# Optimization experiments

Hardware: AMD Instinct MI355X
Metric: run time of the kernel (lower is better)

Reference implementation:

```python
import jax, jax.numpy as jnp
import numpy as np

N = 100000   # nodes
E = 1600000  # edges
D = 128      # input feature dim
H1, H2 = 128, 128    # GCN hidden sizes
M1, M2 = 256, 128    # MLP hidden sizes
BN_EPS = 1e-5


def setup_inputs() -> dict:
    key = jax.random.key(0)
    ks = jax.random.split(key, 20)
    x = jax.random.normal(ks[0], (N, D), dtype=jnp.float32)
    edge_index = jax.random.randint(ks[1], (2, E), 0, N, dtype=jnp.int32)

    def lin(k, fi, fo):
        s = 1.0 / np.sqrt(fi)
        return jax.random.uniform(k, (fi, fo), jnp.float32, -s, s)

    inp = {"x": x, "edge_index": edge_index}
    inp["Wg1"] = lin(ks[2], D, H1);  inp["bg1"] = jnp.zeros((H1,), jnp.float32)
    inp["g1"]  = jnp.ones((H1,), jnp.float32); inp["be1"] = jnp.zeros((H1,), jnp.float32)
    inp["Wg2"] = lin(ks[3], H1, H2); inp["bg2"] = jnp.zeros((H2,), jnp.float32)
    inp["g2"]  = jnp.ones((H2,), jnp.float32); inp["be2"] = jnp.zeros((H2,), jnp.float32)
    inp["Wm1"] = lin(ks[4], H2, M1); inp["bm1"] = jnp.zeros((M1,), jnp.float32)
    inp["g3"]  = jnp.ones((M1,), jnp.float32); inp["be3"] = jnp.zeros((M1,), jnp.float32)
    inp["Wm2"] = lin(ks[5], M1, M2); inp["bm2"] = jnp.zeros((M2,), jnp.float32)
    inp["g4"]  = jnp.ones((M2,), jnp.float32); inp["be4"] = jnp.zeros((M2,), jnp.float32)
    inp["Wo"]  = lin(ks[6], M2, 1);  inp["bo"]  = jnp.zeros((1,), jnp.float32)
    return inp


def batch_norm(x, gamma, beta):
    # training-mode BatchNorm1d over the node/batch axis, biased variance
    mean = jnp.mean(x, axis=0)
    var = jnp.mean((x - mean) ** 2, axis=0)
    return (x - mean) * jax.lax.rsqrt(var + BN_EPS) * gamma + beta


def gcn_conv(x, src, dst, W, b):
    # PyG GCNConv: add self-loops, sym-normalize, aggregate (xW) over edges
    h = x @ W                                              # [N, F_out]
    deg = jnp.zeros((N,), x.dtype).at[dst].add(1.0) + 1.0  # in-degree + self-loop
    dinv = jax.lax.rsqrt(deg)
    coef = (dinv[src] * dinv[dst])[:, None]                # [E, 1]
    agg = jax.ops.segment_sum(h[src] * coef, dst, num_segments=N)
    agg = agg + h * (dinv * dinv)[:, None]                 # self-loop term
    return agg + b


def reference(x, edge_index, Wg1, bg1, g1, be1, Wg2, bg2, g2, be2,
              Wm1, bm1, g3, be3, Wm2, bm2, g4, be4, Wo, bo):
    src, dst = edge_index[0], edge_index[1]
    # GCN blocks: relu(dropout(bn(conv(x)))); dropout is identity in eval
    h = jax.nn.relu(batch_norm(gcn_conv(x, src, dst, Wg1, bg1), g1, be1))
    h = jax.nn.relu(batch_norm(gcn_conv(h, src, dst, Wg2, bg2), g2, be2))
    # MLP blocks
    h = jax.nn.relu(batch_norm(h @ Wm1 + bm1, g3, be3))
    h = jax.nn.relu(batch_norm(h @ Wm2 + bm2, g4, be4))
    return jax.nn.sigmoid(h @ Wo + bo)
```

## Files before the change

kernel.cpp:

```cpp
#include <hip/hip_runtime.h>
#include <hip/hip_bf16.h>
#include <math.h>


__global__ void degree_kernel(const int* __restrict__ dst, int* __restrict__ deg, int E) {
    int i = blockIdx.x * blockDim.x + threadIdx.x;
    if (i < E) atomicAdd(&deg[dst[i]], 1);
}

__global__ void dinv_kernel(const int* __restrict__ deg, float* __restrict__ dinv, int N) {
    int i = blockIdx.x * blockDim.x + threadIdx.x;
    if (i < N) dinv[i] = rsqrtf((float)(deg[i] + 1));
}

__global__ void blocksum_kernel(const int* __restrict__ deg, int* __restrict__ bsum, int N) {
    __shared__ int sh[256];
    int tid = threadIdx.x;
    int base = blockIdx.x * 1024 + tid * 4;
    int s = 0;
    #pragma unroll
    for (int j = 0; j < 4; ++j) { int idx = base + j; if (idx < N) s += deg[idx]; }
    sh[tid] = s; __syncthreads();
    for (int off = 128; off > 0; off >>= 1) {
        if (tid < off) sh[tid] += sh[tid + off];
        __syncthreads();
    }
    if (tid == 0) bsum[blockIdx.x] = sh[0];
}

__global__ void scan_bsum_kernel(int* bsum, int nb) {
    if (threadIdx.x == 0 && blockIdx.x == 0) {
        int run = 0;
        for (int i = 0; i < nb; ++i) { int v = bsum[i]; bsum[i] = run; run += v; }
    }
}

__global__ void scanwrite_kernel(const int* __restrict__ deg, const int* __restrict__ bsumex,
                                 int* __restrict__ row_ptr, int* __restrict__ cursor,
                                 int N, int Etot) {
    __shared__ int sh[256];
    int tid = threadIdx.x;
    int base = blockIdx.x * 1024 + tid * 4;
    int v[4]; int tsum = 0;
    #pragma unroll
    for (int j = 0; j < 4; ++j) { int idx = base + j; v[j] = (idx < N) ? deg[idx] : 0; tsum += v[j]; }
    sh[tid] = tsum; __syncthreads();
    for (int off = 1; off < 256; off <<= 1) {
        int x = (tid >= off) ? sh[tid - off] : 0;
        __syncthreads();
        sh[tid] += x;
        __syncthreads();
    }
    int run = sh[tid] - tsum + bsumex[blockIdx.x];
    #pragma unroll
    for (int j = 0; j < 4; ++j) {
        int idx = base + j;
        if (idx < N) { row_ptr[idx] = run; cursor[idx] = run; }
        run += v[j];
    }
    if (blockIdx.x == 0 && tid == 0) row_ptr[N] = Etot;
}

__global__ void scatter_kernel(const int* __restrict__ src, const int* __restrict__ dst,
                               int* __restrict__ cursor, int* __restrict__ edge_src, int E) {
    int i = blockIdx.x * blockDim.x + threadIdx.x;
    if (i < E) {
        int d = dst[i];
        int pos = atomicAdd(&cursor[d], 1);
        edge_src[pos] = src[i];
    }
}

template<bool ACT>
__global__ __launch_bounds__(256)
void gemm_kernel(const float* __restrict__ A, const float* __restrict__ W,
                 float* __restrict__ C, int nrows, int K, int FO,
                 const float* __restrict__ scale, const float* __restrict__ shift)
{
    __shared__ float As[32][132];
    __shared__ float Ws[32][132];
    const int tid = threadIdx.x;
    const int row0 = blockIdx.x * 128;
    const int c0 = blockIdx.y * 128;
    const int tx = tid & 15, ty = tid >> 4;
    float acc[8][8];
    #pragma unroll
    for (int i = 0; i < 8; ++i)
        #pragma unroll
        for (int j = 0; j < 8; ++j) acc[i][j] = 0.f;

    for (int k0 = 0; k0 < K; k0 += 32) {
        #pragma unroll
        for (int p = 0; p < 4; ++p) {
            int q = p * 256 + tid;
            int r = q >> 3;
            int kq = (q & 7) * 4;
            int gr = row0 + r;
            float4 v = make_float4(0.f, 0.f, 0.f, 0.f);
            if (gr < nrows) {
                v = *(const float4*)&A[(size_t)gr * K + k0 + kq];
                if (ACT) {
                    float4 sc = *(const float4*)&scale[k0 + kq];
                    float4 sf = *(const float4*)&shift[k0 + kq];
                    v.x = fmaxf(fmaf(v.x, sc.x, sf.x), 0.f);
                    v.y = fmaxf(fmaf(v.y, sc.y, sf.y), 0.f);
                    v.z = fmaxf(fmaf(v.z, sc.z, sf.z), 0.f);
                    v.w = fmaxf(fmaf(v.w, sc.w, sf.w), 0.f);
                }
            }
            As[kq + 0][r] = v.x; As[kq + 1][r] = v.y;
            As[kq + 2][r] = v.z; As[kq + 3][r] = v.w;
        }
        #pragma unroll
        for (int p = 0; p < 4; ++p) {
            int q = p * 256 + tid;
            int r = q >> 5;
            int cq = (q & 31) * 4;
            *(float4*)&Ws[r][cq] = *(const float4*)&W[(size_t)(k0 + r) * FO + c0 + cq];
        }
        __syncthreads();
        #pragma unroll
        for (int kk = 0; kk < 32; ++kk) {
            float4 a0 = *(const float4*)&As[kk][ty * 4];
            float4 a1 = *(const float4*)&As[kk][64 + ty * 4];
            float4 b0 = *(const float4*)&Ws[kk][tx * 4];
            float4 b1 = *(const float4*)&Ws[kk][64 + tx * 4];
            float a[8] = {a0.x, a0.y, a0.z, a0.w, a1.x, a1.y, a1.z, a1.w};
            float b[8] = {b0.x, b0.y, b0.z, b0.w, b1.x, b1.y, b1.z, b1.w};
            #pragma unroll
            for (int i = 0; i < 8; ++i)
                #pragma unroll
                for (int j = 0; j < 8; ++j)
                    acc[i][j] = fmaf(a[i], b[j], acc[i][j]);
        }
        __syncthreads();
    }
    #pragma unroll
    for (int i = 0; i < 8; ++i) {
        int r = (i < 4) ? (ty * 4 + i) : (64 + ty * 4 + i - 4);
        int gr = row0 + r;
        if (gr < nrows) {
            float4 o0 = make_float4(acc[i][0], acc[i][1], acc[i][2], acc[i][3]);
            float4 o1 = make_float4(acc[i][4], acc[i][5], acc[i][6], acc[i][7]);
            *(float4*)&C[(size_t)gr * FO + c0 + tx * 4] = o0;
            *(float4*)&C[(size_t)gr * FO + c0 + 64 + tx * 4] = o1;
        }
    }
}

__global__ void agg_kernel(const float* __restrict__ T, float* __restrict__ Aout,
                           const float* __restrict__ dinv,
                           const int* __restrict__ row_ptr, const int* __restrict__ edge_src,
                           int nrows)
{
    int gw = (blockIdx.x * blockDim.x + threadIdx.x) >> 6;
    int lane = threadIdx.x & 63;
    int nw = (gridDim.x * blockDim.x) >> 6;
    int c = lane * 2;
    for (int i = gw; i < nrows; i += nw) {
        float di = dinv[i];
        int e0 = row_ptr[i], e1 = row_ptr[i + 1];
        float ax = 0.f, ay = 0.f;
        for (int e = e0; e < e1; ++e) {
            int s = edge_src[e];
            float ws = dinv[s];
            float2 v = *(const float2*)&T[(size_t)s * 128 + c];
            ax = fmaf(ws, v.x, ax);
            ay = fmaf(ws, v.y, ay);
        }
        float2 self = *(const float2*)&T[(size_t)i * 128 + c];
        float2 o;
        o.x = fmaf(di, ax, di * di * self.x);
        o.y = fmaf(di, ay, di * di * self.y);
        *(float2*)&Aout[(size_t)i * 128 + c] = o;
    }
}

__global__ void colstats_kernel(const float* __restrict__ X, int nrows, int F, int rpb,
                                float* __restrict__ colsum, float* __restrict__ colsq)
{
    __shared__ float ss[256], sq[256];
    int tid = threadIdx.x;
    int c = tid & (F - 1);
    int roff = tid / F;
    int rstep = 256 / F;
    int r0 = blockIdx.x * rpb;
    int r1 = min(nrows, r0 + rpb);
    float s = 0.f, q = 0.f;
    for (int r = r0 + roff; r < r1; r += rstep) {
        float v = X[(size_t)r * F + c];
        s += v; q += v * v;
    }
    ss[tid] = s; sq[tid] = q;
    __syncthreads();
    if (tid < F) {
        float S = ss[tid], Q = sq[tid];
        for (int k = tid + F; k < 256; k += F) { S += ss[k]; Q += sq[k]; }
        atomicAdd(&colsum[tid], S);
        atomicAdd(&colsq[tid], Q);
    }
}

__global__ void bnparam_kernel(const float* __restrict__ colsum, const float* __restrict__ colsq,
                               const float* __restrict__ g, const float* __restrict__ be,
                               float* __restrict__ scale, float* __restrict__ shift,
                               int F, float invN)
{
    int c = blockIdx.x * blockDim.x + threadIdx.x;
    if (c < F) {
        float mean = colsum[c] * invN;
        float var = colsq[c] * invN - mean * mean;
        float rs = rsqrtf(var + 1e-5f);
        float sc = g[c] * rs;
        scale[c] = sc;
        shift[c] = be[c] - mean * sc;
    }
}

__global__ void final_kernel(const float* __restrict__ A, const float* __restrict__ Wo,
                             const float* __restrict__ bo,
                             const float* __restrict__ scale, const float* __restrict__ shift,
                             float* __restrict__ out, int nrows)
{
    int gw = (blockIdx.x * blockDim.x + threadIdx.x) >> 6;
    int lane = threadIdx.x & 63;
    int nw = (gridDim.x * blockDim.x) >> 6;
    int c = lane * 2;
    float2 w = *(const float2*)&Wo[c];
    float2 sc = *(const float2*)&scale[c];
    float2 sf = *(const float2*)&shift[c];
    float bias = bo[0];
    for (int i = gw; i < nrows; i += nw) {
        float2 v = *(const float2*)&A[(size_t)i * 128 + c];
        float x = fmaxf(fmaf(v.x, sc.x, sf.x), 0.f) * w.x
                + fmaxf(fmaf(v.y, sc.y, sf.y), 0.f) * w.y;
        #pragma unroll
        for (int off = 32; off > 0; off >>= 1) x += __shfl_down(x, off);
        if (lane == 0) out[i] = 1.f / (1.f + expf(-(x + bias)));
    }
}

extern "C" void kernel_launch(void* const* d_in, const int* in_sizes, int n_in,
                              void* d_out, int out_size, void* d_ws, size_t ws_size,
                              hipStream_t stream)
{
    const float* x   = (const float*)d_in[0];
    const int* ei    = (const int*)d_in[1];
    const float* Wg1 = (const float*)d_in[2];
    const float* g1  = (const float*)d_in[4];
    const float* be1 = (const float*)d_in[5];
    const float* Wg2 = (const float*)d_in[6];
    const float* g2  = (const float*)d_in[8];
    const float* be2 = (const float*)d_in[9];
    const float* Wm1 = (const float*)d_in[10];
    const float* g3  = (const float*)d_in[12];
    const float* be3 = (const float*)d_in[13];
    const float* Wm2 = (const float*)d_in[14];
    const float* g4  = (const float*)d_in[16];
    const float* be4 = (const float*)d_in[17];
    const float* Wo  = (const float*)d_in[18];
    const float* bo  = (const float*)d_in[19];

    const int N = in_sizes[0] / 128;
    const int E = in_sizes[1] / 2;
    const int* srcv = ei;
    const int* dstv = ei + E;

    char* p = (char*)d_ws;
    auto alloc = [&](size_t bytes) { void* r = (void*)p; p += (bytes + 255) & ~(size_t)255; return r; };
    float* T       = (float*)alloc((size_t)N * 256 * 4);
    float* Abuf    = (float*)alloc((size_t)N * 128 * 4);
    int*   deg     = (int*)alloc((size_t)N * 4);
    float* dinv    = (float*)alloc((size_t)N * 4);
    int*   row_ptr = (int*)alloc((size_t)(N + 1) * 4);
    int*   cursor  = (int*)alloc((size_t)N * 4);
    int*   edge_src= (int*)alloc((size_t)E * 4);
    int*   bsum    = (int*)alloc(4096);
    float* colsum  = (float*)alloc(512 * 4);
    float* colsq   = colsum + 256;
    float* scale   = (float*)alloc(256 * 4);
    float* shift   = (float*)alloc(256 * 4);

    const int rpb = (N + 255) / 256;
    const float invN = 1.f / (float)N;

    hipMemsetAsync(deg, 0, (size_t)N * 4, stream);
    degree_kernel<<<(E + 255) / 256, 256, 0, stream>>>(dstv, deg, E);
    dinv_kernel<<<(N + 255) / 256, 256, 0, stream>>>(deg, dinv, N);
    int nb = (N + 1023) / 1024;
    blocksum_kernel<<<nb, 256, 0, stream>>>(deg, bsum, N);
    scan_bsum_kernel<<<1, 64, 0, stream>>>(bsum, nb);
    scanwrite_kernel<<<nb, 256, 0, stream>>>(deg, bsum, row_ptr, cursor, N, E);
    scatter_kernel<<<(E + 255) / 256, 256, 0, stream>>>(srcv, dstv, cursor, edge_src, E);

    dim3 gemm_g((N + 127) / 128, 1);
    dim3 gemm_g2((N + 127) / 128, 2);

    gemm_kernel<false><<<gemm_g, 256, 0, stream>>>(x, Wg1, T, N, 128, 128, nullptr, nullptr);
    agg_kernel<<<2048, 256, 0, stream>>>(T, Abuf, dinv, row_ptr, edge_src, N);
    hipMemsetAsync(colsum, 0, 512 * 4, stream);
    colstats_kernel<<<256, 256, 0, stream>>>(Abuf, N, 128, rpb, colsum, colsq);
    bnparam_kernel<<<1, 256, 0, stream>>>(colsum, colsq, g1, be1, scale, shift, 128, invN);

    gemm_kernel<true><<<gemm_g, 256, 0, stream>>>(Abuf, Wg2, T, N, 128, 128, scale, shift);
    agg_kernel<<<2048, 256, 0, stream>>>(T, Abuf, dinv, row_ptr, edge_src, N);
    hipMemsetAsync(colsum, 0, 512 * 4, stream);
    colstats_kernel<<<256, 256, 0, stream>>>(Abuf, N, 128, rpb, colsum, colsq);
    bnparam_kernel<<<1, 256, 0, stream>>>(colsum, colsq, g2, be2, scale, shift, 128, invN);

    gemm_kernel<true><<<gemm_g2, 256, 0, stream>>>(Abuf, Wm1, T, N, 128, 256, scale, shift);
    hipMemsetAsync(colsum, 0, 512 * 4, stream);
    colstats_kernel<<<256, 256, 0, stream>>>(T, N, 256, rpb, colsum, colsq);
    bnparam_kernel<<<1, 256, 0, stream>>>(colsum, colsq, g3, be3, scale, shift, 256, invN);

    gemm_kernel<true><<<gemm_g, 256, 0, stream>>>(T, Wm2, Abuf, N, 256, 128, scale, shift);
    hipMemsetAsync(colsum, 0, 512 * 4, stream);
    colstats_kernel<<<256, 256, 0, stream>>>(Abuf, N, 128, rpb, colsum, colsq);
    bnparam_kernel<<<1, 256, 0, stream>>>(colsum, colsq, g4, be4, scale, shift, 128, invN);

    final_kernel<<<1024, 256, 0, stream>>>(Abuf, Wo, bo, scale, shift, (float*)d_out, N);
}
```

Before: 1.230 ms.

## Use split-bf16 MFMA for GEMMs and batch edge loads in aggregation

Replaces the FP32 SIMT GEMM with a matrix-core kernel that splits each FP32 operand into high and low bf16 parts and issues three MFMAs per tile (hh, hl, lh) to keep near-FP32 accuracy. Weights are pre-split and re-laid out by a small per-layer kernel, and activations are split while being staged into LDS. The aggregation kernel now loads 64 edge indices and weights cooperatively per wave and broadcasts them with shuffles, issuing four gathers at a time to raise memory-level parallelism. Costs include extra split arithmetic, scalar uncoalesced output stores, and a small accuracy loss from the dropped low-low term.

```diff
diff --git a/kernel.cpp b/kernel.cpp
--- a/kernel.cpp
+++ b/kernel.cpp
@@ -2,6 +2,20 @@
 #include <hip/hip_bf16.h>
 #include <math.h>
 
+
+typedef __attribute__((ext_vector_type(8))) short bf16x8;
+typedef __attribute__((ext_vector_type(4))) float f32x4;
+
+__device__ inline void split_bf16(float x, ushort& h, ushort& l) {
+    union { float f; unsigned u; } a; a.f = x;
+    unsigned r = (a.u + 0x7FFFu + ((a.u >> 16) & 1u)) >> 16;
+    h = (ushort)r;
+    union { unsigned u; float f; } hb; hb.u = r << 16;
+    float lo = x - hb.f;
+    union { float f; unsigned u; } b; b.f = lo;
+    unsigned r2 = (b.u + 0x7FFFu + ((b.u >> 16) & 1u)) >> 16;
+    l = (ushort)r2;
+}
 
 __global__ void degree_kernel(const int* __restrict__ dst, int* __restrict__ deg, int E) {
     int i = blockIdx.x * blockDim.x + threadIdx.x;
@@ -71,29 +85,55 @@
     }
 }
 
+__global__ void wsplit_kernel(const float* __restrict__ W, ushort* __restrict__ Wh,
+                              ushort* __restrict__ Wl, int K, int FO) {
+    int t = blockIdx.x * 256 + threadIdx.x;
+    if (t >= K * FO) return;
+    int j   = t & 7;
+    int ci  = (t >> 3) & 127;
+    int rest = t >> 10;
+    int nkg = K >> 3;
+    int kg  = rest % nkg;
+    int cb  = rest / nkg;
+    float w = W[(size_t)(kg * 8 + j) * FO + cb * 128 + ci];
+    ushort h, l; split_bf16(w, h, l);
+    Wh[t] = h; Wl[t] = l;
+}
+
+#define AIDX(kg, r, j) ((kg) * 1032 + (r) * 8 + (j))
+
 template<bool ACT>
 __global__ __launch_bounds__(256)
-void gemm_kernel(const float* __restrict__ A, const float* __restrict__ W,
-                 float* __restrict__ C, int nrows, int K, int FO,
-                 const float* __restrict__ scale, const float* __restrict__ shift)
-{
-    __shared__ float As[32][132];
-    __shared__ float Ws[32][132];
-    const int tid = threadIdx.x;
+void gemm_mfma_kernel(const float* __restrict__ A, const ushort* __restrict__ W2h,
+                      const ushort* __restrict__ W2l, float* __restrict__ C,
+                      int nrows, int K, int FO,
+                      const float* __restrict__ scale, const float* __restrict__ shift)
+{
+    __shared__ ushort AsH[4 * 1032 + 8];
+    __shared__ ushort AsL[4 * 1032 + 8];
+    const int tid  = threadIdx.x;
+    const int lane = tid & 63;
+    const int wid  = tid >> 6;
+    const int wm   = wid & 1, wn = wid >> 1;
     const int row0 = blockIdx.x * 128;
-    const int c0 = blockIdx.y * 128;
-    const int tx = tid & 15, ty = tid >> 4;
-    float acc[8][8];
-    #pragma unroll
-    for (int i = 0; i < 8; ++i)
-        #pragma unroll
-        for (int j = 0; j < 8; ++j) acc[i][j] = 0.f;
+    const int cb   = blockIdx.y;
+    const int c0   = cb * 128;
+    const int nkg  = K >> 3;
+    const int l15  = lane & 15;
+    const int l4   = lane >> 4;
+
+    f32x4 zero = {0.f, 0.f, 0.f, 0.f};
+    f32x4 acc[4][4];
+    #pragma unroll
+    for (int m = 0; m < 4; ++m)
+        #pragma unroll
+        for (int n = 0; n < 4; ++n) acc[m][n] = zero;
 
     for (int k0 = 0; k0 < K; k0 += 32) {
         #pragma unroll
         for (int p = 0; p < 4; ++p) {
-            int q = p * 256 + tid;
-            int r = q >> 3;
+            int q  = p * 256 + tid;
+            int r  = q >> 3;
             int kq = (q & 7) * 4;
             int gr = row0 + r;
             float4 v = make_float4(0.f, 0.f, 0.f, 0.f);
@@ -108,42 +148,58 @@
                     v.w = fmaxf(fmaf(v.w, sc.w, sf.w), 0.f);
                 }
             }
-            As[kq + 0][r] = v.x; As[kq + 1][r] = v.y;
-            As[kq + 2][r] = v.z; As[kq + 3][r] = v.w;
-        }
-        #pragma unroll
-        for (int p = 0; p < 4; ++p) {
-            int q = p * 256 + tid;
-            int r = q >> 5;
-            int cq = (q & 31) * 4;
-            *(float4*)&Ws[r][cq] = *(const float4*)&W[(size_t)(k0 + r) * FO + c0 + cq];
-        }
-        __syncthreads();
-        #pragma unroll
-        for (int kk = 0; kk < 32; ++kk) {
-            float4 a0 = *(const float4*)&As[kk][ty * 4];
-            float4 a1 = *(const float4*)&As[kk][64 + ty * 4];
-            float4 b0 = *(const float4*)&Ws[kk][tx * 4];
-            float4 b1 = *(const float4*)&Ws[kk][64 + tx * 4];
-            float a[8] = {a0.x, a0.y, a0.z, a0.w, a1.x, a1.y, a1.z, a1.w};
-            float b[8] = {b0.x, b0.y, b0.z, b0.w, b1.x, b1.y, b1.z, b1.w};
+            ushort h[4], l[4];
+            split_bf16(v.x, h[0], l[0]); split_bf16(v.y, h[1], l[1]);
+            split_bf16(v.z, h[2], l[2]); split_bf16(v.w, h[3], l[3]);
+            int idx = AIDX(kq >> 3, r, kq & 7);
+            union { uint2 u; ushort s[4]; } ph, pl;
+            ph.s[0] = h[0]; ph.s[1] = h[1]; ph.s[2] = h[2]; ph.s[3] = h[3];
+            pl.s[0] = l[0]; pl.s[1] = l[1]; pl.s[2] = l[2]; pl.s[3] = l[3];
+            *(uint2*)&AsH[idx] = ph.u;
+            *(uint2*)&AsL[idx] = pl.u;
+        }
+        __syncthreads();
+
+        const int kgbase = k0 >> 3;
+        bf16x8 bh[4], bl[4];
+        #pragma unroll
+        for (int n = 0; n < 4; ++n) {
+            int ci = wn * 64 + n * 16 + l15;
+            size_t off = (((size_t)(cb * nkg + kgbase + l4)) * 128 + ci) * 8;
+            bh[n] = *(const bf16x8*)&W2h[off];
+            bl[n] = *(const bf16x8*)&W2l[off];
+        }
+        bf16x8 ah[4], al[4];
+        #pragma unroll
+        for (int m = 0; m < 4; ++m) {
+            int idx = AIDX(l4, wm * 64 + m * 16 + l15, 0);
+            ah[m] = *(const bf16x8*)&AsH[idx];
+            al[m] = *(const bf16x8*)&AsL[idx];
+        }
+        #pragma unroll
+        for (int m = 0; m < 4; ++m)
             #pragma unroll
-            for (int i = 0; i < 8; ++i)
+            for (int n = 0; n < 4; ++n) {
+                acc[m][n] = __builtin_amdgcn_mfma_f32_16x16x32_bf16(ah[m], bh[n], acc[m][n], 0, 0, 0);
+                acc[m][n] = __builtin_amdgcn_mfma_f32_16x16x32_bf16(ah[m], bl[n], acc[m][n], 0, 0, 0);
+                acc[m][n] = __builtin_amdgcn_mfma_f32_16x16x32_bf16(al[m], bh[n], acc[m][n], 0, 0, 0);
+            }
+        __syncthreads();
+    }
+
+    #pragma unroll
+    for (int m = 0; m < 4; ++m) {
+        int rbase = row0 + wm * 64 + m * 16 + l4 * 4;
+        #pragma unroll
+        for (int r = 0; r < 4; ++r) {
+            int gr = rbase + r;
+            if (gr < nrows) {
                 #pragma unroll
-                for (int j = 0; j < 8; ++j)
-                    acc[i][j] = fmaf(a[i], b[j], acc[i][j]);
-        }
-        __syncthreads();
-    }
-    #pragma unroll
-    for (int i = 0; i < 8; ++i) {
-        int r = (i < 4) ? (ty * 4 + i) : (64 + ty * 4 + i - 4);
-        int gr = row0 + r;
-        if (gr < nrows) {
-            float4 o0 = make_float4(acc[i][0], acc[i][1], acc[i][2], acc[i][3]);
-            float4 o1 = make_float4(acc[i][4], acc[i][5], acc[i][6], acc[i][7]);
-            *(float4*)&C[(size_t)gr * FO + c0 + tx * 4] = o0;
-            *(float4*)&C[(size_t)gr * FO + c0 + 64 + tx * 4] = o1;
+                for (int n = 0; n < 4; ++n) {
+                    int gc = c0 + wn * 64 + n * 16 + l15;
+                    C[(size_t)gr * FO + gc] = acc[m][n][r];
+                }
+            }
         }
     }
 }
@@ -161,12 +217,26 @@
         float di = dinv[i];
         int e0 = row_ptr[i], e1 = row_ptr[i + 1];
         float ax = 0.f, ay = 0.f;
-        for (int e = e0; e < e1; ++e) {
-            int s = edge_src[e];
-            float ws = dinv[s];
-            float2 v = *(const float2*)&T[(size_t)s * 128 + c];
-            ax = fmaf(ws, v.x, ax);
-            ay = fmaf(ws, v.y, ay);
+        for (int ch = e0; ch < e1; ch += 64) {
+            int rem = e1 - ch;
+            int es = i; float w = 0.f;
+            if (lane < rem) { es = edge_src[ch + lane]; w = dinv[es]; }
+            int cnt = min(rem, 64);
+            int rcnt = (cnt + 3) & ~3;
+            for (int j = 0; j < rcnt; j += 4) {
+                int   s0 = __shfl(es, j),     s1 = __shfl(es, j + 1);
+                int   s2 = __shfl(es, j + 2), s3 = __shfl(es, j + 3);
+                float w0 = __shfl(w, j),      w1 = __shfl(w, j + 1);
+                float w2 = __shfl(w, j + 2),  w3 = __shfl(w, j + 3);
+                float2 v0 = *(const float2*)&T[(size_t)s0 * 128 + c];
+                float2 v1 = *(const float2*)&T[(size_t)s1 * 128 + c];
+                float2 v2 = *(const float2*)&T[(size_t)s2 * 128 + c];
+                float2 v3 = *(const float2*)&T[(size_t)s3 * 128 + c];
+                ax = fmaf(w0, v0.x, ax); ay = fmaf(w0, v0.y, ay);
+                ax = fmaf(w1, v1.x, ax); ay = fmaf(w1, v1.y, ay);
+                ax = fmaf(w2, v2.x, ax); ay = fmaf(w2, v2.y, ay);
+                ax = fmaf(w3, v3.x, ax); ay = fmaf(w3, v3.y, ay);
+            }
         }
         float2 self = *(const float2*)&T[(size_t)i * 128 + c];
         float2 o;
@@ -280,6 +350,8 @@
     float* colsq   = colsum + 256;
     float* scale   = (float*)alloc(256 * 4);
     float* shift   = (float*)alloc(256 * 4);
+    ushort* W2h    = (ushort*)alloc(32768 * 2);
+    ushort* W2l    = (ushort*)alloc(32768 * 2);
 
     const int rpb = (N + 255) / 256;
     const float invN = 1.f / (float)N;
@@ -293,27 +365,32 @@
     scanwrite_kernel<<<nb, 256, 0, stream>>>(deg, bsum, row_ptr, cursor, N, E);
     scatter_kernel<<<(E + 255) / 256, 256, 0, stream>>>(srcv, dstv, cursor, edge_src, E);
 
-    dim3 gemm_g((N + 127) / 128, 1);
-    dim3 gemm_g2((N + 127) / 128, 2);
-
-    gemm_kernel<false><<<gemm_g, 256, 0, stream>>>(x, Wg1, T, N, 128, 128, nullptr, nullptr);
+    const int gx = (N + 127) / 128;
+    dim3 gemm_g(gx, 1);
+    dim3 gemm_g2(gx, 2);
+
+    wsplit_kernel<<<(128 * 128 + 255) / 256, 256, 0, stream>>>(Wg1, W2h, W2l, 128, 128);
+    gemm_mfma_kernel<false><<<gemm_g, 256, 0, stream>>>(x, W2h, W2l, T, N, 128, 128, nullptr, nullptr);
     agg_kernel<<<2048, 256, 0, stream>>>(T, Abuf, dinv, row_ptr, edge_src, N);
     hipMemsetAsync(colsum, 0, 512 * 4, stream);
     colstats_kernel<<<256, 256, 0, stream>>>(Abuf, N, 128, rpb, colsum, colsq);
     bnparam_kernel<<<1, 256, 0, stream>>>(colsum, colsq, g1, be1, scale, shift, 128, invN);
 
-    gemm_kernel<true><<<gemm_g, 256, 0, stream>>>(Abuf, Wg2, T, N, 128, 128, scale, shift);
+    wsplit_kernel<<<(128 * 128 + 255) / 256, 256, 0, stream>>>(Wg2, W2h, W2l, 128, 128);
+    gemm_mfma_kernel<true><<<gemm_g, 256, 0, stream>>>(Abuf, W2h, W2l, T, N, 128, 128, scale, shift);
     agg_kernel<<<2048, 256, 0, stream>>>(T, Abuf, dinv, row_ptr, edge_src, N);
     hipMemsetAsync(colsum, 0, 512 * 4, stream);
     colstats_kernel<<<256, 256, 0, stream>>>(Abuf, N, 128, rpb, colsum, colsq);
     bnparam_kernel<<<1, 256, 0, stream>>>(colsum, colsq, g2, be2, scale, shift, 128, invN);
 
-    gemm_kernel<true><<<gemm_g2, 256, 0, stream>>>(Abuf, Wm1, T, N, 128, 256, scale, shift);
+    wsplit_kernel<<<(128 * 256 + 255) / 256, 256, 0, stream>>>(Wm1, W2h, W2l, 128, 256);
+    gemm_mfma_kernel<true><<<gemm_g2, 256, 0, stream>>>(Abuf, W2h, W2l, T, N, 128, 256, scale, shift);
     hipMemsetAsync(colsum, 0, 512 * 4, stream);
     colstats_kernel<<<256, 256, 0, stream>>>(T, N, 256, rpb, colsum, colsq);
     bnparam_kernel<<<1, 256, 0, stream>>>(colsum, colsq, g3, be3, scale, shift, 256, invN);
 
-    gemm_kernel<true><<<gemm_g, 256, 0, stream>>>(T, Wm2, Abuf, N, 256, 128, scale, shift);
+    wsplit_kernel<<<(256 * 128 + 255) / 256, 256, 0, stream>>>(Wm2, W2h, W2l, 256, 128);
+    gemm_mfma_kernel<true><<<gemm_g, 256, 0, stream>>>(T, W2h, W2l, Abuf, N, 256, 128, scale, shift);
     hipMemsetAsync(colsum, 0, 512 * 4, stream);
     colstats_kernel<<<256, 256, 0, stream>>>(Abuf, N, 128, rpb, colsum, colsq);
     bnparam_kernel<<<1, 256, 0, stream>>>(colsum, colsq, g4, be4, scale, shift, 128, invN);
```

Result: faster. 1.027 ms (-16.5%).
